# Kernel tuning notes

Measured on AMD Instinct MI355X. Metric: run time of the kernel, lower is better.

## Reference

```python
import jax, jax.numpy as jnp
import numpy as np

BETA = 1.0  # cfg.TRAINING.beta
B, S, D = 128, 256, 1024


def setup_inputs() -> dict:
    key = jax.random.key(0)
    k1, k2, k3 = jax.random.split(key, 3)
    bridges = jax.random.normal(k1, (B, S, D), dtype=jnp.float32)
    # monotone increasing timestamps per row (true_divide-safe: bt>bp>bh)
    b_inx = jnp.arange(B * S, dtype=jnp.int32).reshape(B, S)
    # negative indices: one per positive position j in [1, S-2];
    # (idx + 1 + r) % dim guarantees neg_i != i and neg_j != j
    neg_i = (jnp.arange(B, dtype=jnp.int32)[:, None] + 1
             + jax.random.randint(k2, (B, S - 2), 0, B - 1, dtype=jnp.int32)) % B
    neg_j = (jnp.arange(1, S - 1, dtype=jnp.int32)[None, :] + 1
             + jax.random.randint(k3, (B, S - 2), 0, S - 1, dtype=jnp.int32)) % S
    return {"bridges": bridges, "b_inx": b_inx, "neg_i": neg_i, "neg_j": neg_j}


def reference(bridges, b_inx, neg_i, neg_j):
    dt = bridges.dtype
    t = b_inx.astype(dt)
    th = t[:, :1]            # [B,1] head timestamp
    tt = t[:, -1:]           # [B,1] tail timestamp
    tp = t[:, 1:-1]          # [B,S-2] positive timestamps
    alpha = (tp - th) / (tt - th)          # [B,S-2]
    sigma = alpha * (tt - tp)              # [B,S-2]

    head = bridges[:, 0]                   # [B,D]
    tail = bridges[:, -1]                  # [B,D]
    pos = bridges[:, 1:-1]                 # [B,S-2,D]
    neg = bridges[neg_i, neg_j]            # [B,S-2,D]

    a = alpha[..., None]
    mix = (1.0 - a) * head[:, None, :] + a * tail[:, None, :]  # [B,S-2,D]
    xp = pos - mix
    xn = neg - mix
    inv = 1.0 / (2.0 * sigma * sigma)
    pos_dis = -jnp.sum(xp * xp, axis=-1) * inv   # -||x||^2 / (2 sigma^2)
    neg_dis = -jnp.sum(xn * xn, axis=-1) * inv

    cur = pos_dis - neg_dis + jnp.asarray(BETA, dt)
    loss = jnp.sum(jnp.where(cur > 0, cur, jnp.zeros((), dt)))
    return loss / bridges.shape[0]
```

## Files before the change

### kernel.cpp

```cpp
#include <hip/hip_runtime.h>
#include <math.h>

constexpr int   Bc   = 128;
constexpr int   Sc   = 256;
constexpr int   Dc   = 1024;
constexpr float BETA = 1.0f;
constexpr int   SP   = Sc - 2;
constexpr int   NP   = Bc * SP;
constexpr int   NR   = Bc * Sc;
constexpr int   CAP  = 8;

constexpr size_t OFF_CNT  = 0;
constexpr size_t OFF_REC  = 131072;
constexpr size_t OFF_PPAR = OFF_REC + (size_t)NR * CAP * 16;
constexpr size_t OFF_PD   = OFF_PPAR + (size_t)NP * 8;
constexpr size_t OFF_ND   = OFF_PD + (size_t)NP * 4;

__global__ __launch_bounds__(256) void k_build(
    const int* __restrict__ b_inx, const int* __restrict__ neg_i,
    const int* __restrict__ neg_j, int* __restrict__ cnt,
    float4* __restrict__ rec, float2* __restrict__ ppar,
    float* __restrict__ neg_dis, float* __restrict__ out)
{
    const int p = blockIdx.x * 256 + threadIdx.x;
    if (p == 0) out[0] = 0.0f;
    const int b = p / SP;
    const int j = p - b * SP;
    const int s = j + 1;
    const float th = (float)b_inx[b * Sc];
    const float tt = (float)b_inx[b * Sc + (Sc - 1)];
    const float tp = (float)b_inx[b * Sc + s];
    const float alpha = (tp - th) / (tt - th);
    const float sigma = alpha * (tt - tp);
    const float inv   = 1.0f / (2.0f * sigma * sigma);
    ppar[p] = make_float2(alpha, inv);
    const int r = neg_i[p] * Sc + neg_j[p];
    const int slot = atomicAdd(&cnt[r], 1);
    if (slot < CAP) {
        rec[r * CAP + slot] = make_float4(__int_as_float((b << 8) | j), alpha, inv, 0.0f);
    } else {
        neg_dis[p] = INFINITY;
    }
}

__global__ __launch_bounds__(256) void k_main(
    const float* __restrict__ bridges,
    const int* __restrict__ cnt, const float4* __restrict__ rec,
    const float2* __restrict__ ppar,
    float* __restrict__ pos_dis, float* __restrict__ neg_dis)
{
    const int r    = (blockIdx.x * 256 + threadIdx.x) >> 6;
    const int lane = threadIdx.x & 63;
    const int b    = r >> 8;
    const int s    = r & 255;

    const float4* __restrict__ row4 = (const float4*)bridges;

    float4 x[4];
    {
        const float4* rp = row4 + (size_t)r * (Dc / 4);
#pragma unroll
        for (int k = 0; k < 4; ++k) x[k] = rp[k * 64 + lane];
    }

    const int nneg = min(cnt[r], CAP);
    float4 rc = rec[r * CAP];

    const float4* hp = row4 + (size_t)(b * Sc) * (Dc / 4);
    const float4* tq = row4 + (size_t)(b * Sc + Sc - 1) * (Dc / 4);

    if (s >= 1 && s <= Sc - 2) {
        const float2 pp    = ppar[b * SP + (s - 1)];
        const float  alpha = pp.x, inv = pp.y;
        float d = 0.0f;
#pragma unroll
        for (int k = 0; k < 4; ++k) {
            const float4 h = hp[k * 64 + lane];
            const float4 t = tq[k * 64 + lane];
            const float m0 = fmaf(alpha, t.x - h.x, h.x);
            const float m1 = fmaf(alpha, t.y - h.y, h.y);
            const float m2 = fmaf(alpha, t.z - h.z, h.z);
            const float m3 = fmaf(alpha, t.w - h.w, h.w);
            const float e0 = x[k].x - m0, e1 = x[k].y - m1;
            const float e2 = x[k].z - m2, e3 = x[k].w - m3;
            d += e0 * e0 + e1 * e1 + e2 * e2 + e3 * e3;
        }
#pragma unroll
        for (int m = 32; m >= 1; m >>= 1) d += __shfl_xor(d, m);
        if (lane == 0) pos_dis[b * SP + (s - 1)] = -d * inv;
    }

    for (int q = 0; q < nneg; ++q) {
        const int   e     = __float_as_int(rc.x);
        const float alpha = rc.y, inv = rc.z;
        const int   bb = e >> 8;
        const int   jj = e & 255;
        const float4* hb = row4 + (size_t)(bb * Sc) * (Dc / 4);
        const float4* tb = row4 + (size_t)(bb * Sc + Sc - 1) * (Dc / 4);
        if (q + 1 < nneg) rc = rec[r * CAP + q + 1];
        float d = 0.0f;
#pragma unroll
        for (int k = 0; k < 4; ++k) {
            const float4 h = hb[k * 64 + lane];
            const float4 t = tb[k * 64 + lane];
            const float m0 = fmaf(alpha, t.x - h.x, h.x);
            const float m1 = fmaf(alpha, t.y - h.y, h.y);
            const float m2 = fmaf(alpha, t.z - h.z, h.z);
            const float m3 = fmaf(alpha, t.w - h.w, h.w);
            const float e0 = x[k].x - m0, e1 = x[k].y - m1;
            const float e2 = x[k].z - m2, e3 = x[k].w - m3;
            d += e0 * e0 + e1 * e1 + e2 * e2 + e3 * e3;
        }
#pragma unroll
        for (int m = 32; m >= 1; m >>= 1) d += __shfl_xor(d, m);
        if (lane == 0) neg_dis[bb * SP + jj] = -d * inv;
    }
}

__global__ __launch_bounds__(256) void k_hinge(
    const float* __restrict__ bridges, const int* __restrict__ b_inx,
    const int* __restrict__ neg_i, const int* __restrict__ neg_j,
    const float* __restrict__ pos_dis, const float* __restrict__ neg_dis,
    float* __restrict__ out)
{
    float a = 0.0f;
    for (int p = blockIdx.x * 256 + threadIdx.x; p < NP; p += gridDim.x * 256) {
        float nd = neg_dis[p];
        if (__builtin_isinf(nd)) {
            const int bb = p / SP, jj = p - bb * SP, ss = jj + 1;
            const int r  = neg_i[p] * Sc + neg_j[p];
            const float th = (float)b_inx[bb * Sc];
            const float tt = (float)b_inx[bb * Sc + (Sc - 1)];
            const float tp = (float)b_inx[bb * Sc + ss];
            const float alpha = (tp - th) / (tt - th);
            const float sigma = alpha * (tt - tp);
            const float inv   = 1.0f / (2.0f * sigma * sigma);
            const float* xr = bridges + (size_t)r * Dc;
            const float* hr = bridges + (size_t)(bb * Sc) * Dc;
            const float* tr = bridges + (size_t)(bb * Sc + Sc - 1) * Dc;
            float d = 0.0f;
            for (int k = 0; k < Dc; ++k) {
                const float h = hr[k];
                const float m = fmaf(alpha, tr[k] - h, h);
                const float e = xr[k] - m;
                d += e * e;
            }
            nd = -d * inv;
        }
        const float cur = pos_dis[p] - nd + BETA;
        if (cur > 0.0f) a += cur;
    }
    __shared__ float red[4];
#pragma unroll
    for (int m = 32; m >= 1; m >>= 1) a += __shfl_xor(a, m);
    if ((threadIdx.x & 63) == 0) red[threadIdx.x >> 6] = a;
    __syncthreads();
    if (threadIdx.x == 0) {
        const float ssum = red[0] + red[1] + red[2] + red[3];
        atomicAdd(out, ssum * (1.0f / (float)Bc));
    }
}

extern "C" void kernel_launch(void* const* d_in, const int* in_sizes, int n_in,
                              void* d_out, int out_size, void* d_ws, size_t ws_size,
                              hipStream_t stream) {
    const float* bridges = (const float*)d_in[0];
    const int*   b_inx   = (const int*)d_in[1];
    const int*   neg_i   = (const int*)d_in[2];
    const int*   neg_j   = (const int*)d_in[3];
    float*       out     = (float*)d_out;

    char* ws = (char*)d_ws;
    int*    cnt     = (int*)(ws + OFF_CNT);
    float4* rec     = (float4*)(ws + OFF_REC);
    float2* ppar    = (float2*)(ws + OFF_PPAR);
    float*  pos_dis = (float*)(ws + OFF_PD);
    float*  neg_dis = (float*)(ws + OFF_ND);

    hipMemsetAsync(cnt, 0, NR * sizeof(int), stream);
    k_build<<<NP / 256, 256, 0, stream>>>(b_inx, neg_i, neg_j, cnt, rec, ppar, neg_dis, out);
    k_main <<<NR / 4, 256, 0, stream>>>(bridges, cnt, rec, ppar, pos_dis, neg_dis);
    k_hinge<<<128, 256, 0, stream>>>(bridges, b_inx, neg_i, neg_j, pos_dis, neg_dis, out);
}
```

Measured before the change: 208.0 us.

## Process eight rows per wave, caching head/tail deltas and prefetching next row

Each wave now handles eight consecutive rows of one batch instead of a single row. It loads the head row and the tail-minus-head delta once into registers and reuses them for every positive distance, and prefetches the next row while computing the current one. The grid shrinks by a factor of eight, and the launch bounds request four blocks per CU. The hinge kernel also skips its atomic add when a block's sum is zero. The trade-off is fewer waves in flight and higher register pressure, which may reduce latency hiding for the gather-heavy negative loop.

```diff
diff --git a/kernel.cpp b/kernel.cpp
--- a/kernel.cpp
+++ b/kernel.cpp
@@ -9,6 +9,7 @@
 constexpr int   NP   = Bc * SP;
 constexpr int   NR   = Bc * Sc;
 constexpr int   CAP  = 8;
+constexpr int   RPW  = 8;
 
 constexpr size_t OFF_CNT  = 0;
 constexpr size_t OFF_REC  = 131072;
@@ -43,77 +44,102 @@
     }
 }
 
-__global__ __launch_bounds__(256) void k_main(
+__global__ __launch_bounds__(256, 4) void k_main(
     const float* __restrict__ bridges,
     const int* __restrict__ cnt, const float4* __restrict__ rec,
     const float2* __restrict__ ppar,
     float* __restrict__ pos_dis, float* __restrict__ neg_dis)
 {
-    const int r    = (blockIdx.x * 256 + threadIdx.x) >> 6;
+    const int wid  = (blockIdx.x * 256 + threadIdx.x) >> 6;
     const int lane = threadIdx.x & 63;
-    const int b    = r >> 8;
-    const int s    = r & 255;
+    const int b    = wid >> 5;
+    const int c    = wid & 31;
+    const int r0   = b * Sc + c * RPW;
 
     const float4* __restrict__ row4 = (const float4*)bridges;
 
-    float4 x[4];
+    float4 h[4], dt[4];
     {
-        const float4* rp = row4 + (size_t)r * (Dc / 4);
-#pragma unroll
-        for (int k = 0; k < 4; ++k) x[k] = rp[k * 64 + lane];
-    }
-
-    const int nneg = min(cnt[r], CAP);
-    float4 rc = rec[r * CAP];
-
-    const float4* hp = row4 + (size_t)(b * Sc) * (Dc / 4);
-    const float4* tq = row4 + (size_t)(b * Sc + Sc - 1) * (Dc / 4);
-
-    if (s >= 1 && s <= Sc - 2) {
-        const float2 pp    = ppar[b * SP + (s - 1)];
-        const float  alpha = pp.x, inv = pp.y;
-        float d = 0.0f;
+        const float4* hp = row4 + (size_t)(b * Sc) * (Dc / 4);
+        const float4* tp = row4 + (size_t)(b * Sc + Sc - 1) * (Dc / 4);
 #pragma unroll
         for (int k = 0; k < 4; ++k) {
-            const float4 h = hp[k * 64 + lane];
-            const float4 t = tq[k * 64 + lane];
-            const float m0 = fmaf(alpha, t.x - h.x, h.x);
-            const float m1 = fmaf(alpha, t.y - h.y, h.y);
-            const float m2 = fmaf(alpha, t.z - h.z, h.z);
-            const float m3 = fmaf(alpha, t.w - h.w, h.w);
-            const float e0 = x[k].x - m0, e1 = x[k].y - m1;
-            const float e2 = x[k].z - m2, e3 = x[k].w - m3;
-            d += e0 * e0 + e1 * e1 + e2 * e2 + e3 * e3;
-        }
-#pragma unroll
-        for (int m = 32; m >= 1; m >>= 1) d += __shfl_xor(d, m);
-        if (lane == 0) pos_dis[b * SP + (s - 1)] = -d * inv;
-    }
-
-    for (int q = 0; q < nneg; ++q) {
-        const int   e     = __float_as_int(rc.x);
-        const float alpha = rc.y, inv = rc.z;
-        const int   bb = e >> 8;
-        const int   jj = e & 255;
-        const float4* hb = row4 + (size_t)(bb * Sc) * (Dc / 4);
-        const float4* tb = row4 + (size_t)(bb * Sc + Sc - 1) * (Dc / 4);
-        if (q + 1 < nneg) rc = rec[r * CAP + q + 1];
-        float d = 0.0f;
-#pragma unroll
-        for (int k = 0; k < 4; ++k) {
-            const float4 h = hb[k * 64 + lane];
-            const float4 t = tb[k * 64 + lane];
-            const float m0 = fmaf(alpha, t.x - h.x, h.x);
-            const float m1 = fmaf(alpha, t.y - h.y, h.y);
-            const float m2 = fmaf(alpha, t.z - h.z, h.z);
-            const float m3 = fmaf(alpha, t.w - h.w, h.w);
-            const float e0 = x[k].x - m0, e1 = x[k].y - m1;
-            const float e2 = x[k].z - m2, e3 = x[k].w - m3;
-            d += e0 * e0 + e1 * e1 + e2 * e2 + e3 * e3;
-        }
-#pragma unroll
-        for (int m = 32; m >= 1; m >>= 1) d += __shfl_xor(d, m);
-        if (lane == 0) neg_dis[bb * SP + jj] = -d * inv;
+            h[k] = hp[k * 64 + lane];
+            const float4 t = tp[k * 64 + lane];
+            dt[k] = make_float4(t.x - h[k].x, t.y - h[k].y, t.z - h[k].z, t.w - h[k].w);
+        }
+    }
+
+    float4 xc[4], xn[4];
+    {
+        const float4* rp = row4 + (size_t)r0 * (Dc / 4);
+#pragma unroll
+        for (int k = 0; k < 4; ++k) xc[k] = rp[k * 64 + lane];
+    }
+
+    for (int i = 0; i < RPW; ++i) {
+        const int r = r0 + i;
+        const int s = c * RPW + i;
+
+        if (i + 1 < RPW) {
+            const float4* rp = row4 + (size_t)(r + 1) * (Dc / 4);
+#pragma unroll
+            for (int k = 0; k < 4; ++k) xn[k] = rp[k * 64 + lane];
+        }
+
+        const int nneg = min(cnt[r], CAP);
+        float4 rc = rec[r * CAP];
+
+        if (s >= 1 && s <= Sc - 2) {
+            const float2 pp    = ppar[b * SP + (s - 1)];
+            const float  alpha = pp.x, inv = pp.y;
+            float d = 0.0f;
+#pragma unroll
+            for (int k = 0; k < 4; ++k) {
+                const float m0 = fmaf(alpha, dt[k].x, h[k].x);
+                const float m1 = fmaf(alpha, dt[k].y, h[k].y);
+                const float m2 = fmaf(alpha, dt[k].z, h[k].z);
+                const float m3 = fmaf(alpha, dt[k].w, h[k].w);
+                const float e0 = xc[k].x - m0, e1 = xc[k].y - m1;
+                const float e2 = xc[k].z - m2, e3 = xc[k].w - m3;
+                d += e0 * e0 + e1 * e1 + e2 * e2 + e3 * e3;
+            }
+#pragma unroll
+            for (int m = 32; m >= 1; m >>= 1) d += __shfl_xor(d, m);
+            if (lane == 0) pos_dis[b * SP + (s - 1)] = -d * inv;
+        }
+
+        for (int q = 0; q < nneg; ++q) {
+            const int   e     = __float_as_int(rc.x);
+            const float alpha = rc.y, inv = rc.z;
+            const int   bb = e >> 8;
+            const int   jj = e & 255;
+            const float4* hb = row4 + (size_t)(bb * Sc) * (Dc / 4);
+            const float4* tb = row4 + (size_t)(bb * Sc + Sc - 1) * (Dc / 4);
+            if (q + 1 < nneg) rc = rec[r * CAP + q + 1];
+            float d = 0.0f;
+#pragma unroll
+            for (int half = 0; half < 2; ++half) {
+#pragma unroll
+                for (int k = half * 2; k < half * 2 + 2; ++k) {
+                    const float4 hh = hb[k * 64 + lane];
+                    const float4 tt = tb[k * 64 + lane];
+                    const float m0 = fmaf(alpha, tt.x - hh.x, hh.x);
+                    const float m1 = fmaf(alpha, tt.y - hh.y, hh.y);
+                    const float m2 = fmaf(alpha, tt.z - hh.z, hh.z);
+                    const float m3 = fmaf(alpha, tt.w - hh.w, hh.w);
+                    const float e0 = xc[k].x - m0, e1 = xc[k].y - m1;
+                    const float e2 = xc[k].z - m2, e3 = xc[k].w - m3;
+                    d += e0 * e0 + e1 * e1 + e2 * e2 + e3 * e3;
+                }
+            }
+#pragma unroll
+            for (int m = 32; m >= 1; m >>= 1) d += __shfl_xor(d, m);
+            if (lane == 0) neg_dis[bb * SP + jj] = -d * inv;
+        }
+
+#pragma unroll
+        for (int k = 0; k < 4; ++k) xc[k] = xn[k];
     }
 }
 
@@ -157,7 +183,7 @@
     __syncthreads();
     if (threadIdx.x == 0) {
         const float ssum = red[0] + red[1] + red[2] + red[3];
-        atomicAdd(out, ssum * (1.0f / (float)Bc));
+        if (ssum != 0.0f) atomicAdd(out, ssum * (1.0f / (float)Bc));
     }
 }
 
@@ -179,6 +205,6 @@
 
     hipMemsetAsync(cnt, 0, NR * sizeof(int), stream);
     k_build<<<NP / 256, 256, 0, stream>>>(b_inx, neg_i, neg_j, cnt, rec, ppar, neg_dis, out);
-    k_main <<<NR / 4, 256, 0, stream>>>(bridges, cnt, rec, ppar, pos_dis, neg_dis);
+    k_main <<<NR / (64 / 64 * 4 * RPW), 256, 0, stream>>>(bridges, cnt, rec, ppar, pos_dis, neg_dis);
     k_hinge<<<128, 256, 0, stream>>>(bridges, b_inx, neg_i, neg_j, pos_dis, neg_dis, out);
 }
```

After: 218.3 us. 4.9% more time.
